# Kernel tuning notes

Measured on AMD Instinct MI355X. Metric: run time of the kernel, lower is better.

## Reference

```python
import jax, jax.numpy as jnp
import numpy as np

N = 50000      # nodes
E = 800000     # edges
F_IN = 128     # input features
H = 128        # hidden width
C = 64         # classes


def _glorot(key, fan_in, fan_out):
    lim = float(np.sqrt(6.0 / (fan_in + fan_out)))
    return jax.random.uniform(key, (fan_in, fan_out), jnp.float32, -lim, lim)


def setup_inputs() -> dict:
    key = jax.random.key(0)
    ks = jax.random.split(key, 8)
    x = jax.random.normal(ks[0], (N, F_IN), jnp.float32)
    edge_index = jax.random.randint(ks[1], (2, E), 0, N, dtype=jnp.int64)
    return {
        "x": x,
        "edge_index": edge_index,
        "W0": _glorot(ks[2], F_IN, H), "b0": jnp.zeros((H,), jnp.float32),
        "W1": _glorot(ks[3], H, H),    "b1": jnp.zeros((H,), jnp.float32),
        "W2": _glorot(ks[4], H, C),    "b2": jnp.zeros((C,), jnp.float32),
    }


def _gcn_norm(edge_index, n):
    # add self-loops, then symmetric normalization D^-1/2 A D^-1/2
    loop = jnp.arange(n, dtype=edge_index.dtype)
    src = jnp.concatenate([edge_index[0], loop])   # message source j
    dst = jnp.concatenate([edge_index[1], loop])   # aggregation target i
    deg = jax.ops.segment_sum(jnp.ones_like(dst, jnp.float32), dst, num_segments=n)
    dinv = jnp.where(deg > 0, jax.lax.rsqrt(jnp.maximum(deg, 1.0)), 0.0)
    norm = dinv[src] * dinv[dst]                   # [E+N]
    return src, dst, norm


def _gcn_conv(x, W, b, src, dst, norm, n):
    h = x @ W                                      # [N, out]
    msg = norm[:, None] * h[src]                   # gather [E+N, out]
    out = jax.ops.segment_sum(msg, dst, num_segments=n)  # scatter-add
    return out + b


def reference(x, edge_index, W0, b0, W1, b1, W2, b2):
    n = x.shape[0]
    src, dst, norm = _gcn_norm(edge_index, n)
    h = _gcn_conv(x, W0, b0, src, dst, norm, n)
    h = h * jax.nn.sigmoid(h)                      # swish
    h = _gcn_conv(h, W1, b1, src, dst, norm, n)
    h = h * jax.nn.sigmoid(h)
    h = _gcn_conv(h, W2, b2, src, dst, norm, n)
    return jax.nn.log_softmax(h, axis=1)
```

## Files before the change

kernel.cpp:

```cpp
#include <hip/hip_runtime.h>


#define NODES_PER_BUCKET 1024
#define MAX_BUCKETS 64
#define CVT_BLOCKS 160

typedef __attribute__((ext_vector_type(8))) short short8;
typedef __attribute__((ext_vector_type(4))) float f32x4;

__device__ inline unsigned bf16_rn(float x) {
    unsigned u = __float_as_uint(x);
    return (u + 0x7fffu + ((u >> 16) & 1u)) >> 16;
}
__device__ inline float bf_lo(unsigned u) { return __uint_as_float(u << 16); }
__device__ inline float bf_hi(unsigned u) { return __uint_as_float(u & 0xffff0000u); }

__global__ __launch_bounds__(256) void prep_k(const int* __restrict__ dst, int e,
                                              int* __restrict__ bcnt,
                                              const float* __restrict__ W0,
                                              const float* __restrict__ W1,
                                              const float* __restrict__ W2,
                                              unsigned short* __restrict__ Wt) {
    const int t = threadIdx.x;
    if (blockIdx.x < CVT_BLOCKS) {
        int id = blockIdx.x * 256 + t;
        const float* W;
        int out, loc;
        if (id < 16384)      { W = W0; out = 128; loc = id; }
        else if (id < 32768) { W = W1; out = 128; loc = id - 16384; }
        else                 { W = W2; out = 64;  loc = id - 32768; }
        int o = loc >> 7, k = loc & 127;
        Wt[id] = (unsigned short)bf16_rn(W[k * out + o]);
        return;
    }
    __shared__ int h[MAX_BUCKETS];
    if (t < MAX_BUCKETS) h[t] = 0;
    __syncthreads();
    const int i0 = (blockIdx.x - CVT_BLOCKS) * 4096;
#pragma unroll
    for (int k = 0; k < 16; ++k) {
        int i = i0 + t + k * 256;
        if (i < e) atomicAdd(&h[dst[i] >> 10], 1);
    }
    __syncthreads();
    if (t < MAX_BUCKETS && h[t]) atomicAdd(&bcnt[t], h[t]);
}

__global__ __launch_bounds__(512) void scatter_k(const int* __restrict__ src,
                                                 const int* __restrict__ dst,
                                                 int e,
                                                 const int* __restrict__ bcnt,
                                                 int* __restrict__ scur,
                                                 uint2* __restrict__ pairs) {
    __shared__ int bbase_s[MAX_BUCKETS];
    __shared__ int cnt[MAX_BUCKETS];
    __shared__ int cur[MAX_BUCKETS];
    __shared__ int gb[MAX_BUCKETS];
    const int t = threadIdx.x;
    if (t < MAX_BUCKETS) {
        int v = bcnt[t];
        int x = v;
#pragma unroll
        for (int off = 1; off < 64; off <<= 1) {
            int y = __shfl_up(x, off);
            if ((t & 63) >= off) x += y;
        }
        bbase_s[t] = x - v;
        cnt[t] = 0;
    }
    __syncthreads();
    const int i0 = blockIdx.x * 8192;
    int d[16];
#pragma unroll
    for (int k = 0; k < 16; ++k) {
        int i = i0 + t + k * 512;
        d[k] = (i < e) ? dst[i] : -1;
        if (d[k] >= 0) atomicAdd(&cnt[d[k] >> 10], 1);
    }
    __syncthreads();
    if (t < MAX_BUCKETS) {
        gb[t] = cnt[t] ? bbase_s[t] + atomicAdd(&scur[t], cnt[t]) : 0;
        cur[t] = 0;
    }
    __syncthreads();
#pragma unroll
    for (int k = 0; k < 16; ++k) {
        int i = i0 + t + k * 512;
        if (d[k] >= 0) {
            int b = d[k] >> 10;
            int r = atomicAdd(&cur[b], 1);
            pairs[gb[b] + r] = make_uint2((unsigned)src[i], (unsigned)d[k]);
        }
    }
}

__global__ __launch_bounds__(1024) void build_k(const uint2* __restrict__ pairs,
                                                const int* __restrict__ bcnt,
                                                int n, int e,
                                                int* __restrict__ rp,
                                                float* __restrict__ dinv,
                                                int* __restrict__ col) {
    __shared__ int hist[1024];
    __shared__ int tsum[1024];
    __shared__ int sE[2];
    const int t = threadIdx.x;
    const int node0 = blockIdx.x << 10;
    if (t < MAX_BUCKETS) {
        int v = bcnt[t];
        int x = v;
#pragma unroll
        for (int off = 1; off < 64; off <<= 1) {
            int y = __shfl_up(x, off);
            if ((t & 63) >= off) x += y;
        }
        if (t == blockIdx.x) { sE[0] = x - v; sE[1] = x; }
    }
    hist[t] = 0;
    __syncthreads();
    const int ebase = sE[0];
    const int eend = sE[1];
    for (int i = ebase + t; i < eend; i += 1024) {
        uint2 p = pairs[i];
        atomicAdd(&hist[(int)p.y - node0], 1);
    }
    __syncthreads();
    const int deg = hist[t];
    tsum[t] = deg;
    __syncthreads();
    for (int off = 1; off < 1024; off <<= 1) {
        int x = (t >= off) ? tsum[t - off] : 0;
        __syncthreads();
        tsum[t] += x;
        __syncthreads();
    }
    const int excl = tsum[t] - deg;
    if (node0 + t < n) {
        rp[node0 + t] = ebase + excl;
        dinv[node0 + t] = rsqrtf((float)(deg + 1));
    }
    hist[t] = excl;
    __syncthreads();
    for (int i = ebase + t; i < eend; i += 1024) {
        uint2 p = pairs[i];
        int r = atomicAdd(&hist[(int)p.y - node0], 1);
        col[ebase + r] = (int)p.x;
    }
    if (blockIdx.x == 0 && t == 0) rp[n] = e;
}

template <int OUT, bool F32IN>
__global__ __launch_bounds__(256) void mfma_gemm_k(
    const void* __restrict__ Av,
    const unsigned short* __restrict__ Wt,
    const float* __restrict__ dinv,
    unsigned short* __restrict__ G,
    int n) {
    constexpr int NF = OUT / 16;
    __shared__ unsigned short lds[(128 + OUT) * 128];
    unsigned short* As = lds;
    unsigned short* Ws = lds + 128 * 128;

    const int tid = threadIdx.x;
    const int row0 = blockIdx.x * 128;

#pragma unroll
    for (int p = 0; p < 8; ++p) {
        int id = p * 256 + tid;
        int r = id >> 4, c = id & 15;
        uint4 v = make_uint4(0, 0, 0, 0);
        if (row0 + r < n) {
            if (F32IN) {
                const float* Af = (const float*)Av;
                const float4* fp =
                    (const float4*)&Af[(size_t)(row0 + r) * 128 + c * 8];
                float4 v0 = fp[0], v1 = fp[1];
                v.x = bf16_rn(v0.x) | (bf16_rn(v0.y) << 16);
                v.y = bf16_rn(v0.z) | (bf16_rn(v0.w) << 16);
                v.z = bf16_rn(v1.x) | (bf16_rn(v1.y) << 16);
                v.w = bf16_rn(v1.z) | (bf16_rn(v1.w) << 16);
            } else {
                const unsigned short* Ab = (const unsigned short*)Av;
                v = *(const uint4*)&Ab[(size_t)(row0 + r) * 128 + c * 8];
            }
        }
        int bo = r * 256 + ((c * 16) ^ ((r & 7) << 4));
        *(uint4*)((char*)As + bo) = v;
    }
#pragma unroll
    for (int p = 0; p < OUT / 16; ++p) {
        int id = p * 256 + tid;
        int r = id >> 4, c = id & 15;
        uint4 v = *(const uint4*)&Wt[(size_t)r * 128 + c * 8];
        int bo = r * 256 + ((c * 16) ^ ((r & 7) << 4));
        *(uint4*)((char*)Ws + bo) = v;
    }
    __syncthreads();

    const int wid = tid >> 6, lane = tid & 63;
    const int lq = lane >> 4, lr = lane & 15;
    const int woff = wid * 32;

    f32x4 acc[2][NF] = {};
#pragma unroll
    for (int ks = 0; ks < 4; ++ks) {
        short8 a[2];
#pragma unroll
        for (int m = 0; m < 2; ++m) {
            int r = woff + m * 16 + lr;
            int bo = r * 256 + ((lq * 16 + ks * 64) ^ ((r & 7) << 4));
            a[m] = *(const short8*)((const char*)As + bo);
        }
#pragma unroll
        for (int nf = 0; nf < NF; ++nf) {
            int c = nf * 16 + lr;
            int bo = c * 256 + ((lq * 16 + ks * 64) ^ ((c & 7) << 4));
            short8 b = *(const short8*)((const char*)Ws + bo);
            acc[0][nf] = __builtin_amdgcn_mfma_f32_16x16x32_bf16(a[0], b, acc[0][nf], 0, 0, 0);
            acc[1][nf] = __builtin_amdgcn_mfma_f32_16x16x32_bf16(a[1], b, acc[1][nf], 0, 0, 0);
        }
    }

#pragma unroll
    for (int m = 0; m < 2; ++m) {
#pragma unroll
        for (int j = 0; j < 4; ++j) {
            int r = row0 + woff + m * 16 + lq * 4 + j;
            if (r < n) {
                float d = dinv[r];
#pragma unroll
                for (int nf = 0; nf < NF; ++nf)
                    G[(size_t)r * OUT + nf * 16 + lr] =
                        (unsigned short)bf16_rn(d * acc[m][nf][j]);
            }
        }
    }
}

__device__ inline void acc8(float* a, uint4 u) {
    a[0] += bf_lo(u.x); a[1] += bf_hi(u.x);
    a[2] += bf_lo(u.y); a[3] += bf_hi(u.y);
    a[4] += bf_lo(u.z); a[5] += bf_hi(u.z);
    a[6] += bf_lo(u.w); a[7] += bf_hi(u.w);
}

__global__ __launch_bounds__(512, 4) void agg_swish_k(const uint4* __restrict__ G4,
                                                      const int* __restrict__ rp,
                                                      const int* __restrict__ col,
                                                      const float* __restrict__ dinv,
                                                      const float* __restrict__ bias,
                                                      uint4* __restrict__ Hb4, int n) {
    const int i = (blockIdx.x * blockDim.x + threadIdx.x) >> 4;
    const int sl = threadIdx.x & 15;
    if (i >= n) return;

    float a[8] = {0.f, 0.f, 0.f, 0.f, 0.f, 0.f, 0.f, 0.f};
    acc8(a, G4[(size_t)i * 16 + sl]);
    const int s = rp[i], e = rp[i + 1];
    int p = s;
    for (; p + 8 <= e; p += 8) {
        uint4 v[8];
#pragma unroll
        for (int k = 0; k < 8; ++k) {
            int j = col[p + k];
            v[k] = G4[(size_t)j * 16 + sl];
        }
#pragma unroll
        for (int k = 0; k < 8; ++k) acc8(a, v[k]);
    }
    if (p < e) {
        const int m = e - p;
        uint4 v[8];
#pragma unroll
        for (int k = 0; k < 8; ++k) {
            int j = col[min(p + k, e - 1)];
            v[k] = G4[(size_t)j * 16 + sl];
        }
#pragma unroll
        for (int k = 0; k < 8; ++k)
            if (k < m) acc8(a, v[k]);
    }

    const float d = dinv[i];
    const float4 bl = *(const float4*)&bias[sl * 8];
    const float4 bh = *(const float4*)&bias[sl * 8 + 4];
    float r[8];
    r[0] = d * a[0] + bl.x; r[1] = d * a[1] + bl.y;
    r[2] = d * a[2] + bl.z; r[3] = d * a[3] + bl.w;
    r[4] = d * a[4] + bh.x; r[5] = d * a[5] + bh.y;
    r[6] = d * a[6] + bh.z; r[7] = d * a[7] + bh.w;
#pragma unroll
    for (int k = 0; k < 8; ++k) r[k] = r[k] / (1.f + expf(-r[k]));
    uint4 o;
    o.x = bf16_rn(r[0]) | (bf16_rn(r[1]) << 16);
    o.y = bf16_rn(r[2]) | (bf16_rn(r[3]) << 16);
    o.z = bf16_rn(r[4]) | (bf16_rn(r[5]) << 16);
    o.w = bf16_rn(r[6]) | (bf16_rn(r[7]) << 16);
    Hb4[(size_t)i * 16 + sl] = o;
}

__global__ __launch_bounds__(512, 4) void agg_lsm_k(const uint2* __restrict__ G2,
                                                    const int* __restrict__ rp,
                                                    const int* __restrict__ col,
                                                    const float* __restrict__ dinv,
                                                    const float* __restrict__ bias,
                                                    float* __restrict__ out, int n) {
    const int i = (blockIdx.x * blockDim.x + threadIdx.x) >> 4;
    const int sl = threadIdx.x & 15;
    if (i >= n) return;

    float a[4] = {0.f, 0.f, 0.f, 0.f};
    {
        uint2 u = G2[(size_t)i * 16 + sl];
        a[0] += bf_lo(u.x); a[1] += bf_hi(u.x);
        a[2] += bf_lo(u.y); a[3] += bf_hi(u.y);
    }
    const int s = rp[i], e = rp[i + 1];
    int p = s;
    for (; p + 8 <= e; p += 8) {
        uint2 v[8];
#pragma unroll
        for (int k = 0; k < 8; ++k) {
            int j = col[p + k];
            v[k] = G2[(size_t)j * 16 + sl];
        }
#pragma unroll
        for (int k = 0; k < 8; ++k) {
            a[0] += bf_lo(v[k].x); a[1] += bf_hi(v[k].x);
            a[2] += bf_lo(v[k].y); a[3] += bf_hi(v[k].y);
        }
    }
    if (p < e) {
        const int m = e - p;
        uint2 v[8];
#pragma unroll
        for (int k = 0; k < 8; ++k) {
            int j = col[min(p + k, e - 1)];
            v[k] = G2[(size_t)j * 16 + sl];
        }
#pragma unroll
        for (int k = 0; k < 8; ++k)
            if (k < m) {
                a[0] += bf_lo(v[k].x); a[1] += bf_hi(v[k].x);
                a[2] += bf_lo(v[k].y); a[3] += bf_hi(v[k].y);
            }
    }

    const float d = dinv[i];
    const float4 bv = *(const float4*)&bias[sl * 4];
    float lg[4];
    lg[0] = d * a[0] + bv.x; lg[1] = d * a[1] + bv.y;
    lg[2] = d * a[2] + bv.z; lg[3] = d * a[3] + bv.w;

    float m0 = fmaxf(fmaxf(lg[0], lg[1]), fmaxf(lg[2], lg[3]));
#pragma unroll
    for (int off = 1; off < 16; off <<= 1) m0 = fmaxf(m0, __shfl_xor(m0, off));
    float es = expf(lg[0] - m0) + expf(lg[1] - m0) +
               expf(lg[2] - m0) + expf(lg[3] - m0);
#pragma unroll
    for (int off = 1; off < 16; off <<= 1) es += __shfl_xor(es, off);
    const float lse = m0 + logf(es);
    float4 o;
    o.x = lg[0] - lse; o.y = lg[1] - lse; o.z = lg[2] - lse; o.w = lg[3] - lse;
    *(float4*)&out[(size_t)i * 64 + sl * 4] = o;
}

extern "C" void kernel_launch(void* const* d_in, const int* in_sizes, int n_in,
                              void* d_out, int out_size, void* d_ws, size_t ws_size,
                              hipStream_t stream) {
    const float* x = (const float*)d_in[0];
    const int* ei = (const int*)d_in[1];
    const float* W0 = (const float*)d_in[2];
    const float* b0 = (const float*)d_in[3];
    const float* W1 = (const float*)d_in[4];
    const float* b1 = (const float*)d_in[5];
    const float* W2 = (const float*)d_in[6];
    const float* b2 = (const float*)d_in[7];
    float* out = (float*)d_out;

    const int n = in_sizes[0] / 128;
    const int e = in_sizes[1] / 2;
    const int* src = ei;
    const int* dst = ei + e;

    char* ws = (char*)d_ws;
    size_t off = 0;
    auto alloc = [&](size_t bytes) -> void* {
        void* p = ws + off;
        off += (bytes + 255) & ~(size_t)255;
        return p;
    };
    int* bcnt = (int*)alloc(MAX_BUCKETS * 4 * 2);
    int* scur = bcnt + MAX_BUCKETS;
    int* rp = (int*)alloc((size_t)(n + 1) * 4);
    float* dinv = (float*)alloc((size_t)n * 4);
    int* col = (int*)alloc((size_t)e * 4);
    uint2* pairs = (uint2*)alloc((size_t)e * 8);
    unsigned short* wt = (unsigned short*)alloc(40960 * 2);
    unsigned short* g = (unsigned short*)alloc((size_t)n * 256);
    unsigned short* hb = (unsigned short*)alloc((size_t)n * 256);

    unsigned short* w0t = wt;
    unsigned short* w1t = wt + 16384;
    unsigned short* w2t = wt + 32768;

    hipMemsetAsync(bcnt, 0, MAX_BUCKETS * 4 * 2, stream);
    prep_k<<<CVT_BLOCKS + (e + 4095) / 4096, 256, 0, stream>>>(dst, e, bcnt,
                                                               W0, W1, W2, wt);
    scatter_k<<<(e + 8191) / 8192, 512, 0, stream>>>(src, dst, e, bcnt, scur, pairs);
    const int nbuck = (n + NODES_PER_BUCKET - 1) / NODES_PER_BUCKET;
    build_k<<<nbuck, 1024, 0, stream>>>(pairs, bcnt, n, e, rp, dinv, col);

    const int gb = (n + 127) / 128;
    const int ab = (n + 31) / 32;

    mfma_gemm_k<128, true><<<gb, 256, 0, stream>>>(x, w0t, dinv, g, n);
    agg_swish_k<<<ab, 512, 0, stream>>>((const uint4*)g, rp, col, dinv, b0,
                                        (uint4*)hb, n);
    mfma_gemm_k<128, false><<<gb, 256, 0, stream>>>(hb, w1t, dinv, g, n);
    agg_swish_k<<<ab, 512, 0, stream>>>((const uint4*)g, rp, col, dinv, b1,
                                        (uint4*)hb, n);
    mfma_gemm_k<64, false><<<gb, 256, 0, stream>>>(hb, w2t, dinv, g, n);
    agg_lsm_k<<<ab, 512, 0, stream>>>((const uint2*)g, rp, col, dinv, b2, out, n);
}
```

Baseline: 172.4 us.

## Fuse aggregation+swish with next-layer GEMM and pack edge pairs into 32 bits

The separate agg_swish and bf16 GEMM kernels for layers 1 and 2 are merged into one agg_gemm kernel. Each block aggregates 64 nodes into LDS, applies bias and swish, then multiplies by the next weight matrix with MFMA. This removes the global write and re-read of the hidden activations and cuts two kernel launches. Edge pairs are also packed into one 32-bit word (src<<10 | local dst), halving the bucket-sort traffic, which assumes fewer than about 4M nodes. The fused kernel uses smaller 64-row GEMM tiles and more LDS per block, which may lower occupancy during the gather phase.

After: 162.5 us. 1.06x faster.

```diff
diff --git a/kernel.cpp b/kernel.cpp
--- a/kernel.cpp
+++ b/kernel.cpp
@@ -51,7 +51,7 @@
                                                  int e,
                                                  const int* __restrict__ bcnt,
                                                  int* __restrict__ scur,
-                                                 uint2* __restrict__ pairs) {
+                                                 unsigned* __restrict__ pairs) {
     __shared__ int bbase_s[MAX_BUCKETS];
     __shared__ int cnt[MAX_BUCKETS];
     __shared__ int cur[MAX_BUCKETS];
@@ -89,12 +89,12 @@
         if (d[k] >= 0) {
             int b = d[k] >> 10;
             int r = atomicAdd(&cur[b], 1);
-            pairs[gb[b] + r] = make_uint2((unsigned)src[i], (unsigned)d[k]);
-        }
-    }
-}
-
-__global__ __launch_bounds__(1024) void build_k(const uint2* __restrict__ pairs,
+            pairs[gb[b] + r] = ((unsigned)src[i] << 10) | ((unsigned)d[k] & 1023u);
+        }
+    }
+}
+
+__global__ __launch_bounds__(1024) void build_k(const unsigned* __restrict__ pairs,
                                                 const int* __restrict__ bcnt,
                                                 int n, int e,
                                                 int* __restrict__ rp,
@@ -104,7 +104,6 @@
     __shared__ int tsum[1024];
     __shared__ int sE[2];
     const int t = threadIdx.x;
-    const int node0 = blockIdx.x << 10;
     if (t < MAX_BUCKETS) {
         int v = bcnt[t];
         int x = v;
@@ -119,10 +118,8 @@
     __syncthreads();
     const int ebase = sE[0];
     const int eend = sE[1];
-    for (int i = ebase + t; i < eend; i += 1024) {
-        uint2 p = pairs[i];
-        atomicAdd(&hist[(int)p.y - node0], 1);
-    }
+    for (int i = ebase + t; i < eend; i += 1024)
+        atomicAdd(&hist[pairs[i] & 1023u], 1);
     __syncthreads();
     const int deg = hist[t];
     tsum[t] = deg;
@@ -134,6 +131,7 @@
         __syncthreads();
     }
     const int excl = tsum[t] - deg;
+    const int node0 = blockIdx.x << 10;
     if (node0 + t < n) {
         rp[node0 + t] = ebase + excl;
         dinv[node0 + t] = rsqrtf((float)(deg + 1));
@@ -141,22 +139,20 @@
     hist[t] = excl;
     __syncthreads();
     for (int i = ebase + t; i < eend; i += 1024) {
-        uint2 p = pairs[i];
-        int r = atomicAdd(&hist[(int)p.y - node0], 1);
-        col[ebase + r] = (int)p.x;
+        unsigned p = pairs[i];
+        int r = atomicAdd(&hist[p & 1023u], 1);
+        col[ebase + r] = (int)(p >> 10);
     }
     if (blockIdx.x == 0 && t == 0) rp[n] = e;
 }
 
-template <int OUT, bool F32IN>
-__global__ __launch_bounds__(256) void mfma_gemm_k(
-    const void* __restrict__ Av,
+__global__ __launch_bounds__(256) void mfma_gemm0_k(
+    const float* __restrict__ Af,
     const unsigned short* __restrict__ Wt,
     const float* __restrict__ dinv,
     unsigned short* __restrict__ G,
     int n) {
-    constexpr int NF = OUT / 16;
-    __shared__ unsigned short lds[(128 + OUT) * 128];
+    __shared__ unsigned short lds[256 * 128];
     unsigned short* As = lds;
     unsigned short* Ws = lds + 128 * 128;
 
@@ -169,23 +165,143 @@
         int r = id >> 4, c = id & 15;
         uint4 v = make_uint4(0, 0, 0, 0);
         if (row0 + r < n) {
-            if (F32IN) {
-                const float* Af = (const float*)Av;
-                const float4* fp =
-                    (const float4*)&Af[(size_t)(row0 + r) * 128 + c * 8];
-                float4 v0 = fp[0], v1 = fp[1];
-                v.x = bf16_rn(v0.x) | (bf16_rn(v0.y) << 16);
-                v.y = bf16_rn(v0.z) | (bf16_rn(v0.w) << 16);
-                v.z = bf16_rn(v1.x) | (bf16_rn(v1.y) << 16);
-                v.w = bf16_rn(v1.z) | (bf16_rn(v1.w) << 16);
-            } else {
-                const unsigned short* Ab = (const unsigned short*)Av;
-                v = *(const uint4*)&Ab[(size_t)(row0 + r) * 128 + c * 8];
-            }
+            const float4* fp = (const float4*)&Af[(size_t)(row0 + r) * 128 + c * 8];
+            float4 v0 = fp[0], v1 = fp[1];
+            v.x = bf16_rn(v0.x) | (bf16_rn(v0.y) << 16);
+            v.y = bf16_rn(v0.z) | (bf16_rn(v0.w) << 16);
+            v.z = bf16_rn(v1.x) | (bf16_rn(v1.y) << 16);
+            v.w = bf16_rn(v1.z) | (bf16_rn(v1.w) << 16);
         }
         int bo = r * 256 + ((c * 16) ^ ((r & 7) << 4));
         *(uint4*)((char*)As + bo) = v;
     }
+#pragma unroll
+    for (int p = 0; p < 8; ++p) {
+        int id = p * 256 + tid;
+        int r = id >> 4, c = id & 15;
+        uint4 v = *(const uint4*)&Wt[(size_t)r * 128 + c * 8];
+        int bo = r * 256 + ((c * 16) ^ ((r & 7) << 4));
+        *(uint4*)((char*)Ws + bo) = v;
+    }
+    __syncthreads();
+
+    const int wid = tid >> 6, lane = tid & 63;
+    const int lq = lane >> 4, lr = lane & 15;
+    const int woff = wid * 32;
+
+    f32x4 acc[2][8] = {};
+#pragma unroll
+    for (int ks = 0; ks < 4; ++ks) {
+        short8 a[2];
+#pragma unroll
+        for (int m = 0; m < 2; ++m) {
+            int r = woff + m * 16 + lr;
+            int bo = r * 256 + ((lq * 16 + ks * 64) ^ ((r & 7) << 4));
+            a[m] = *(const short8*)((const char*)As + bo);
+        }
+#pragma unroll
+        for (int nf = 0; nf < 8; ++nf) {
+            int c = nf * 16 + lr;
+            int bo = c * 256 + ((lq * 16 + ks * 64) ^ ((c & 7) << 4));
+            short8 b = *(const short8*)((const char*)Ws + bo);
+            acc[0][nf] = __builtin_amdgcn_mfma_f32_16x16x32_bf16(a[0], b, acc[0][nf], 0, 0, 0);
+            acc[1][nf] = __builtin_amdgcn_mfma_f32_16x16x32_bf16(a[1], b, acc[1][nf], 0, 0, 0);
+        }
+    }
+
+#pragma unroll
+    for (int m = 0; m < 2; ++m) {
+#pragma unroll
+        for (int j = 0; j < 4; ++j) {
+            int r = row0 + woff + m * 16 + lq * 4 + j;
+            if (r < n) {
+                float d = dinv[r];
+#pragma unroll
+                for (int nf = 0; nf < 8; ++nf)
+                    G[(size_t)r * 128 + nf * 16 + lr] =
+                        (unsigned short)bf16_rn(d * acc[m][nf][j]);
+            }
+        }
+    }
+}
+
+__device__ inline void acc8(float* a, uint4 u) {
+    a[0] += bf_lo(u.x); a[1] += bf_hi(u.x);
+    a[2] += bf_lo(u.y); a[3] += bf_hi(u.y);
+    a[4] += bf_lo(u.z); a[5] += bf_hi(u.z);
+    a[6] += bf_lo(u.w); a[7] += bf_hi(u.w);
+}
+
+template <int OUT>
+__global__ __launch_bounds__(256, 4) void agg_gemm_k(
+    const uint4* __restrict__ G4,
+    const int* __restrict__ rp,
+    const int* __restrict__ col,
+    const float* __restrict__ dinv,
+    const float* __restrict__ bias,
+    const unsigned short* __restrict__ Wt,
+    unsigned short* __restrict__ Gn,
+    int n) {
+    constexpr int NF = OUT / 16;
+    __shared__ unsigned short lds[(64 + OUT) * 128];
+    unsigned short* As = lds;
+    unsigned short* Ws = lds + 64 * 128;
+
+    const int tid = threadIdx.x;
+    const int base = blockIdx.x * 64;
+    const int sl = tid & 15;
+
+    const float4 bl = *(const float4*)&bias[sl * 8];
+    const float4 bh = *(const float4*)&bias[sl * 8 + 4];
+#pragma unroll
+    for (int q = 0; q < 4; ++q) {
+        const int local = (tid >> 4) + q * 16;
+        const int i = base + local;
+        uint4 o = make_uint4(0, 0, 0, 0);
+        if (i < n) {
+            float a[8] = {0.f, 0.f, 0.f, 0.f, 0.f, 0.f, 0.f, 0.f};
+            acc8(a, G4[(size_t)i * 16 + sl]);
+            const int s = rp[i], e = rp[i + 1];
+            int p = s;
+            for (; p + 8 <= e; p += 8) {
+                uint4 v[8];
+#pragma unroll
+                for (int k = 0; k < 8; ++k) {
+                    int j = col[p + k];
+                    v[k] = G4[(size_t)j * 16 + sl];
+                }
+#pragma unroll
+                for (int k = 0; k < 8; ++k) acc8(a, v[k]);
+            }
+            if (p < e) {
+                const int m = e - p;
+                uint4 v[8];
+#pragma unroll
+                for (int k = 0; k < 8; ++k) {
+                    int j = col[min(p + k, e - 1)];
+                    v[k] = G4[(size_t)j * 16 + sl];
+                }
+#pragma unroll
+                for (int k = 0; k < 8; ++k)
+                    if (k < m) acc8(a, v[k]);
+            }
+            const float d = dinv[i];
+            float r[8];
+            r[0] = d * a[0] + bl.x; r[1] = d * a[1] + bl.y;
+            r[2] = d * a[2] + bl.z; r[3] = d * a[3] + bl.w;
+            r[4] = d * a[4] + bh.x; r[5] = d * a[5] + bh.y;
+            r[6] = d * a[6] + bh.z; r[7] = d * a[7] + bh.w;
+#pragma unroll
+            for (int k = 0; k < 8; ++k) r[k] = r[k] / (1.f + expf(-r[k]));
+            o.x = bf16_rn(r[0]) | (bf16_rn(r[1]) << 16);
+            o.y = bf16_rn(r[2]) | (bf16_rn(r[3]) << 16);
+            o.z = bf16_rn(r[4]) | (bf16_rn(r[5]) << 16);
+            o.w = bf16_rn(r[6]) | (bf16_rn(r[7]) << 16);
+        }
+        int bo = local * 256 + ((sl * 16) ^ ((local & 7) << 4));
+        *(uint4*)((char*)As + bo) = o;
+    }
+
 #pragma unroll
     for (int p = 0; p < OUT / 16; ++p) {
         int id = p * 256 + tid;
@@ -198,104 +314,34 @@
 
     const int wid = tid >> 6, lane = tid & 63;
     const int lq = lane >> 4, lr = lane & 15;
-    const int woff = wid * 32;
-
-    f32x4 acc[2][NF] = {};
+    const int woff = wid * 16;
+
+    f32x4 acc[NF] = {};
 #pragma unroll
     for (int ks = 0; ks < 4; ++ks) {
-        short8 a[2];
-#pragma unroll
-        for (int m = 0; m < 2; ++m) {
-            int r = woff + m * 16 + lr;
-            int bo = r * 256 + ((lq * 16 + ks * 64) ^ ((r & 7) << 4));
-            a[m] = *(const short8*)((const char*)As + bo);
-        }
+        int r = woff + lr;
+        int bo = r * 256 + ((lq * 16 + ks * 64) ^ ((r & 7) << 4));
+        short8 a = *(const short8*)((const char*)As + bo);
 #pragma unroll
         for (int nf = 0; nf < NF; ++nf) {
             int c = nf * 16 + lr;
-            int bo = c * 256 + ((lq * 16 + ks * 64) ^ ((c & 7) << 4));
-            short8 b = *(const short8*)((const char*)Ws + bo);
-            acc[0][nf] = __builtin_amdgcn_mfma_f32_16x16x32_bf16(a[0], b, acc[0][nf], 0, 0, 0);
-            acc[1][nf] = __builtin_amdgcn_mfma_f32_16x16x32_bf16(a[1], b, acc[1][nf], 0, 0, 0);
-        }
-    }
-
-#pragma unroll
-    for (int m = 0; m < 2; ++m) {
-#pragma unroll
-        for (int j = 0; j < 4; ++j) {
-            int r = row0 + woff + m * 16 + lq * 4 + j;
-            if (r < n) {
-                float d = dinv[r];
-#pragma unroll
-                for (int nf = 0; nf < NF; ++nf)
-                    G[(size_t)r * OUT + nf * 16 + lr] =
-                        (unsigned short)bf16_rn(d * acc[m][nf][j]);
-            }
-        }
-    }
-}
-
-__device__ inline void acc8(float* a, uint4 u) {
-    a[0] += bf_lo(u.x); a[1] += bf_hi(u.x);
-    a[2] += bf_lo(u.y); a[3] += bf_hi(u.y);
-    a[4] += bf_lo(u.z); a[5] += bf_hi(u.z);
-    a[6] += bf_lo(u.w); a[7] += bf_hi(u.w);
-}
-
-__global__ __launch_bounds__(512, 4) void agg_swish_k(const uint4* __restrict__ G4,
-                                                      const int* __restrict__ rp,
-                                                      const int* __restrict__ col,
-                                                      const float* __restrict__ dinv,
-                                                      const float* __restrict__ bias,
-                                                      uint4* __restrict__ Hb4, int n) {
-    const int i = (blockIdx.x * blockDim.x + threadIdx.x) >> 4;
-    const int sl = threadIdx.x & 15;
-    if (i >= n) return;
-
-    float a[8] = {0.f, 0.f, 0.f, 0.f, 0.f, 0.f, 0.f, 0.f};
-    acc8(a, G4[(size_t)i * 16 + sl]);
-    const int s = rp[i], e = rp[i + 1];
-    int p = s;
-    for (; p + 8 <= e; p += 8) {
-        uint4 v[8];
-#pragma unroll
-        for (int k = 0; k < 8; ++k) {
-            int j = col[p + k];
-            v[k] = G4[(size_t)j * 16 + sl];
-        }
-#pragma unroll
-        for (int k = 0; k < 8; ++k) acc8(a, v[k]);
-    }
-    if (p < e) {
-        const int m = e - p;
-        uint4 v[8];
-#pragma unroll
-        for (int k = 0; k < 8; ++k) {
-            int j = col[min(p + k, e - 1)];
-            v[k] = G4[(size_t)j * 16 + sl];
-        }
-#pragma unroll
-        for (int k = 0; k < 8; ++k)
-            if (k < m) acc8(a, v[k]);
-    }
-
-    const float d = dinv[i];
-    const float4 bl = *(const float4*)&bias[sl * 8];
-    const float4 bh = *(const float4*)&bias[sl * 8 + 4];
-    float r[8];
-    r[0] = d * a[0] + bl.x; r[1] = d * a[1] + bl.y;
-    r[2] = d * a[2] + bl.z; r[3] = d * a[3] + bl.w;
-    r[4] = d * a[4] + bh.x; r[5] = d * a[5] + bh.y;
-    r[6] = d * a[6] + bh.z; r[7] = d * a[7] + bh.w;
-#pragma unroll
-    for (int k = 0; k < 8; ++k) r[k] = r[k] / (1.f + expf(-r[k]));
-    uint4 o;
-    o.x = bf16_rn(r[0]) | (bf16_rn(r[1]) << 16);
-    o.y = bf16_rn(r[2]) | (bf16_rn(r[3]) << 16);
-    o.z = bf16_rn(r[4]) | (bf16_rn(r[5]) << 16);
-    o.w = bf16_rn(r[6]) | (bf16_rn(r[7]) << 16);
-    Hb4[(size_t)i * 16 + sl] = o;
+            int wo = c * 256 + ((lq * 16 + ks * 64) ^ ((c & 7) << 4));
+            short8 b = *(const short8*)((const char*)Ws + wo);
+            acc[nf] = __builtin_amdgcn_mfma_f32_16x16x32_bf16(a, b, acc[nf], 0, 0, 0);
+        }
+    }
+
+#pragma unroll
+    for (int j = 0; j < 4; ++j) {
+        int r = base + woff + lq * 4 + j;
+        if (r < n) {
+            float d = dinv[r];
+#pragma unroll
+            for (int nf = 0; nf < NF; ++nf)
+                Gn[(size_t)r * OUT + nf * 16 + lr] =
+                    (unsigned short)bf16_rn(d * acc[nf][j]);
+        }
+    }
 }
 
 __global__ __launch_bounds__(512, 4) void agg_lsm_k(const uint2* __restrict__ G2,
@@ -394,10 +440,10 @@
     int* rp = (int*)alloc((size_t)(n + 1) * 4);
     float* dinv = (float*)alloc((size_t)n * 4);
     int* col = (int*)alloc((size_t)e * 4);
-    uint2* pairs = (uint2*)alloc((size_t)e * 8);
+    unsigned* pairs = (unsigned*)alloc((size_t)e * 4);
     unsigned short* wt = (unsigned short*)alloc(40960 * 2);
-    unsigned short* g = (unsigned short*)alloc((size_t)n * 256);
-    unsigned short* hb = (unsigned short*)alloc((size_t)n * 256);
+    unsigned short* ga = (unsigned short*)alloc((size_t)n * 256);
+    unsigned short* gb = (unsigned short*)alloc((size_t)n * 256);
 
     unsigned short* w0t = wt;
     unsigned short* w1t = wt + 16384;
@@ -410,15 +456,14 @@
     const int nbuck = (n + NODES_PER_BUCKET - 1) / NODES_PER_BUCKET;
     build_k<<<nbuck, 1024, 0, stream>>>(pairs, bcnt, n, e, rp, dinv, col);
 
-    const int gb = (n + 127) / 128;
+    const int gb128 = (n + 127) / 128;
+    const int fb = (n + 63) / 64;
     const int ab = (n + 31) / 32;
 
-    mfma_gemm_k<128, true><<<gb, 256, 0, stream>>>(x, w0t, dinv, g, n);
-    agg_swish_k<<<ab, 512, 0, stream>>>((const uint4*)g, rp, col, dinv, b0,
-                                        (uint4*)hb, n);
-    mfma_gemm_k<128, false><<<gb, 256, 0, stream>>>(hb, w1t, dinv, g, n);
-    agg_swish_k<<<ab, 512, 0, stream>>>((const uint4*)g, rp, col, dinv, b1,
-                                        (uint4*)hb, n);
-    mfma_gemm_k<64, false><<<gb, 256, 0, stream>>>(hb, w2t, dinv, g, n);
-    agg_lsm_k<<<ab, 512, 0, stream>>>((const uint2*)g, rp, col, dinv, b2, out, n);
-}
+    mfma_gemm0_k<<<gb128, 256, 0, stream>>>(x, w0t, dinv, ga, n);
+    agg_gemm_k<128><<<fb, 256, 0, stream>>>((const uint4*)ga, rp, col, dinv, b0,
+                                            w1t, gb, n);
+    agg_gemm_k<64><<<fb, 256, 0, stream>>>((const uint4*)gb, rp, col, dinv, b1,
+                                           w2t, ga, n);
+    agg_lsm_k<<<ab, 512, 0, stream>>>((const uint2*)ga, rp, col, dinv, b2, out, n);
+}
```

## Pack edge pairs and CSR columns into narrower ints; slice aggregation by feature quarter

Applied to the files above, without the earlier changes.

Edge pairs are now one 32-bit word, holding the source index shifted left 10 bits plus the destination's offset within its bucket. CSR column indices are stored as 16-bit values. This halves pair and column memory traffic in the build and in every aggregation pass. The swish aggregation kernel is restructured so each block covers 64 nodes and one quarter of the feature columns, with 4 lanes per node, to change gather locality and occupancy. The 16-bit columns only work while the node count stays below 65536, and the finer feature split issues more, smaller gathers per edge.

New measurement: 172.6 us. About the same (+0.1%).

```diff
diff --git a/kernel.cpp b/kernel.cpp
--- a/kernel.cpp
+++ b/kernel.cpp
@@ -51,7 +51,7 @@
                                                  int e,
                                                  const int* __restrict__ bcnt,
                                                  int* __restrict__ scur,
-                                                 uint2* __restrict__ pairs) {
+                                                 unsigned* __restrict__ pairs) {
     __shared__ int bbase_s[MAX_BUCKETS];
     __shared__ int cnt[MAX_BUCKETS];
     __shared__ int cur[MAX_BUCKETS];
@@ -89,22 +89,21 @@
         if (d[k] >= 0) {
             int b = d[k] >> 10;
             int r = atomicAdd(&cur[b], 1);
-            pairs[gb[b] + r] = make_uint2((unsigned)src[i], (unsigned)d[k]);
-        }
-    }
-}
-
-__global__ __launch_bounds__(1024) void build_k(const uint2* __restrict__ pairs,
+            pairs[gb[b] + r] = ((unsigned)src[i] << 10) | ((unsigned)d[k] & 1023u);
+        }
+    }
+}
+
+__global__ __launch_bounds__(1024) void build_k(const unsigned* __restrict__ pairs,
                                                 const int* __restrict__ bcnt,
                                                 int n, int e,
                                                 int* __restrict__ rp,
                                                 float* __restrict__ dinv,
-                                                int* __restrict__ col) {
+                                                unsigned short* __restrict__ col) {
     __shared__ int hist[1024];
     __shared__ int tsum[1024];
     __shared__ int sE[2];
     const int t = threadIdx.x;
-    const int node0 = blockIdx.x << 10;
     if (t < MAX_BUCKETS) {
         int v = bcnt[t];
         int x = v;
@@ -119,10 +118,8 @@
     __syncthreads();
     const int ebase = sE[0];
     const int eend = sE[1];
-    for (int i = ebase + t; i < eend; i += 1024) {
-        uint2 p = pairs[i];
-        atomicAdd(&hist[(int)p.y - node0], 1);
-    }
+    for (int i = ebase + t; i < eend; i += 1024)
+        atomicAdd(&hist[pairs[i] & 1023u], 1);
     __syncthreads();
     const int deg = hist[t];
     tsum[t] = deg;
@@ -134,6 +131,7 @@
         __syncthreads();
     }
     const int excl = tsum[t] - deg;
+    const int node0 = blockIdx.x << 10;
     if (node0 + t < n) {
         rp[node0 + t] = ebase + excl;
         dinv[node0 + t] = rsqrtf((float)(deg + 1));
@@ -141,9 +139,9 @@
     hist[t] = excl;
     __syncthreads();
     for (int i = ebase + t; i < eend; i += 1024) {
-        uint2 p = pairs[i];
-        int r = atomicAdd(&hist[(int)p.y - node0], 1);
-        col[ebase + r] = (int)p.x;
+        unsigned p = pairs[i];
+        int r = atomicAdd(&hist[p & 1023u], 1);
+        col[ebase + r] = (unsigned short)(p >> 10);
     }
     if (blockIdx.x == 0 && t == 0) rp[n] = e;
 }
@@ -243,18 +241,22 @@
     a[6] += bf_lo(u.w); a[7] += bf_hi(u.w);
 }
 
-__global__ __launch_bounds__(512, 4) void agg_swish_k(const uint4* __restrict__ G4,
-                                                      const int* __restrict__ rp,
-                                                      const int* __restrict__ col,
-                                                      const float* __restrict__ dinv,
-                                                      const float* __restrict__ bias,
-                                                      uint4* __restrict__ Hb4, int n) {
-    const int i = (blockIdx.x * blockDim.x + threadIdx.x) >> 4;
-    const int sl = threadIdx.x & 15;
+__global__ __launch_bounds__(256, 4) void agg_swish_sl_k(
+    const uint4* __restrict__ G4,
+    const int* __restrict__ rp,
+    const unsigned short* __restrict__ col,
+    const float* __restrict__ dinv,
+    const float* __restrict__ bias,
+    uint4* __restrict__ H4,
+    int n) {
+    const int sl = blockIdx.x & 3;
+    const int i = (blockIdx.x >> 2) * 64 + (threadIdx.x >> 2);
+    const int q = threadIdx.x & 3;
     if (i >= n) return;
+    const int off = sl * 4 + q;
 
     float a[8] = {0.f, 0.f, 0.f, 0.f, 0.f, 0.f, 0.f, 0.f};
-    acc8(a, G4[(size_t)i * 16 + sl]);
+    acc8(a, G4[(size_t)i * 16 + off]);
     const int s = rp[i], e = rp[i + 1];
     int p = s;
     for (; p + 8 <= e; p += 8) {
@@ -262,7 +264,7 @@
 #pragma unroll
         for (int k = 0; k < 8; ++k) {
             int j = col[p + k];
-            v[k] = G4[(size_t)j * 16 + sl];
+            v[k] = G4[(size_t)j * 16 + off];
         }
 #pragma unroll
         for (int k = 0; k < 8; ++k) acc8(a, v[k]);
@@ -273,7 +275,7 @@
 #pragma unroll
         for (int k = 0; k < 8; ++k) {
             int j = col[min(p + k, e - 1)];
-            v[k] = G4[(size_t)j * 16 + sl];
+            v[k] = G4[(size_t)j * 16 + off];
         }
 #pragma unroll
         for (int k = 0; k < 8; ++k)
@@ -281,8 +283,9 @@
     }
 
     const float d = dinv[i];
-    const float4 bl = *(const float4*)&bias[sl * 8];
-    const float4 bh = *(const float4*)&bias[sl * 8 + 4];
+    const int c0 = off * 8;
+    const float4 bl = *(const float4*)&bias[c0];
+    const float4 bh = *(const float4*)&bias[c0 + 4];
     float r[8];
     r[0] = d * a[0] + bl.x; r[1] = d * a[1] + bl.y;
     r[2] = d * a[2] + bl.z; r[3] = d * a[3] + bl.w;
@@ -295,12 +298,12 @@
     o.y = bf16_rn(r[2]) | (bf16_rn(r[3]) << 16);
     o.z = bf16_rn(r[4]) | (bf16_rn(r[5]) << 16);
     o.w = bf16_rn(r[6]) | (bf16_rn(r[7]) << 16);
-    Hb4[(size_t)i * 16 + sl] = o;
+    H4[(size_t)i * 16 + off] = o;
 }
 
 __global__ __launch_bounds__(512, 4) void agg_lsm_k(const uint2* __restrict__ G2,
                                                     const int* __restrict__ rp,
-                                                    const int* __restrict__ col,
+                                                    const unsigned short* __restrict__ col,
                                                     const float* __restrict__ dinv,
                                                     const float* __restrict__ bias,
                                                     float* __restrict__ out, int n) {
@@ -393,10 +396,11 @@
     int* scur = bcnt + MAX_BUCKETS;
     int* rp = (int*)alloc((size_t)(n + 1) * 4);
     float* dinv = (float*)alloc((size_t)n * 4);
-    int* col = (int*)alloc((size_t)e * 4);
-    uint2* pairs = (uint2*)alloc((size_t)e * 8);
+    unsigned short* col = (unsigned short*)alloc((size_t)e * 2);
+    unsigned* pairs = (unsigned*)alloc((size_t)e * 4);
     unsigned short* wt = (unsigned short*)alloc(40960 * 2);
-    unsigned short* g = (unsigned short*)alloc((size_t)n * 256);
+    unsigned short* ga = (unsigned short*)alloc((size_t)n * 256);
+    unsigned short* gbuf = (unsigned short*)alloc((size_t)n * 256);
     unsigned short* hb = (unsigned short*)alloc((size_t)n * 256);
 
     unsigned short* w0t = wt;
@@ -410,15 +414,16 @@
     const int nbuck = (n + NODES_PER_BUCKET - 1) / NODES_PER_BUCKET;
     build_k<<<nbuck, 1024, 0, stream>>>(pairs, bcnt, n, e, rp, dinv, col);
 
-    const int gb = (n + 127) / 128;
+    const int gb128 = (n + 127) / 128;
+    const int sb = 4 * ((n + 63) / 64);
     const int ab = (n + 31) / 32;
 
-    mfma_gemm_k<128, true><<<gb, 256, 0, stream>>>(x, w0t, dinv, g, n);
-    agg_swish_k<<<ab, 512, 0, stream>>>((const uint4*)g, rp, col, dinv, b0,
-                                        (uint4*)hb, n);
-    mfma_gemm_k<128, false><<<gb, 256, 0, stream>>>(hb, w1t, dinv, g, n);
-    agg_swish_k<<<ab, 512, 0, stream>>>((const uint4*)g, rp, col, dinv, b1,
-                                        (uint4*)hb, n);
-    mfma_gemm_k<64, false><<<gb, 256, 0, stream>>>(hb, w2t, dinv, g, n);
-    agg_lsm_k<<<ab, 512, 0, stream>>>((const uint2*)g, rp, col, dinv, b2, out, n);
-}
+    mfma_gemm_k<128, true><<<gb128, 256, 0, stream>>>(x, w0t, dinv, ga, n);
+    agg_swish_sl_k<<<sb, 256, 0, stream>>>((const uint4*)ga, rp, col, dinv, b0,
+                                           (uint4*)hb, n);
+    mfma_gemm_k<128, false><<<gb128, 256, 0, stream>>>(hb, w1t, dinv, gbuf, n);
+    agg_swish_sl_k<<<sb, 256, 0, stream>>>((const uint4*)gbuf, rp, col, dinv, b1,
+                                           (uint4*)hb, n);
+    mfma_gemm_k<64, false><<<gb128, 256, 0, stream>>>(hb, w2t, dinv, ga, n);
+    agg_lsm_k<<<ab, 512, 0, stream>>>((const uint2*)ga, rp, col, dinv, b2, out, n);
+}
```
